# Performance work log

Hardware: AMD Instinct MI355X
Metric: run time of the kernel (lower is better)

The kernel has to match this reference:

```python
import jax, jax.numpy as jnp
import numpy as np

B = 8192
N_INPUT = 64
N_OUTPUT = 128
N_HIDDEN = 32
N_TARGETS = 2
N_EXOGS = 3
N_SERIES = N_TARGETS + N_EXOGS  # 5


def _init_linear(k, fan_in, w_shape, b_shape):
    # torch nn.Linear default init: U(-1/sqrt(fan_in), 1/sqrt(fan_in))
    bound = 1.0 / np.sqrt(fan_in)
    kw, kb = jax.random.split(k)
    W = jax.random.uniform(kw, w_shape, jnp.float32, -bound, bound)
    b = jax.random.uniform(kb, b_shape, jnp.float32, -bound, bound)
    return W, b


def setup_inputs() -> dict:
    key = jax.random.key(0)
    ks = jax.random.split(key, 5)
    target = jax.random.normal(ks[0], (B, N_INPUT, N_TARGETS), jnp.float32)
    exog = jax.random.normal(ks[1], (B, N_INPUT + N_OUTPUT, N_EXOGS), jnp.float32)
    # linear1: (n_input*n_series) -> n_targets
    W1, b1 = _init_linear(ks[2], N_INPUT * N_SERIES, (N_TARGETS, N_INPUT * N_SERIES), (N_TARGETS,))
    # linear2: n_series separate (n_input -> n_hidden) linears, stacked
    W2, b2 = _init_linear(ks[3], N_INPUT, (N_SERIES, N_HIDDEN, N_INPUT), (N_SERIES, N_HIDDEN))
    # linear3: (n_hidden*n_series) -> n_targets
    W3, b3 = _init_linear(ks[4], N_HIDDEN * N_SERIES, (N_TARGETS, N_HIDDEN * N_SERIES), (N_TARGETS,))
    return dict(target=target, exog=exog, W1=W1, b1=b1, W2=W2, b2=b2, W3=W3, b3=b3)


def _single_predict(window, ex, W1, b1, W2, b2, W3, b3):
    # window: (B, n_input, n_targets), ex: (B, n_input, n_exogs)
    te = jnp.concatenate([window, ex], axis=2)  # (B, n_input, n_series)
    flat = te.reshape(te.shape[0], -1)          # time-major, series fastest (torch Flatten order)
    out1 = flat @ W1.T + b1                     # (B, n_targets)
    # per-series tiny linears batched via einsum: h[b,i,:] = W2[i] @ te[b,:,i]
    h = jnp.einsum('bti,iht->bih', te, W2) + b2  # (B, n_series, n_hidden)
    h = jax.nn.sigmoid(h).reshape(h.shape[0], -1)  # series-major concat order matches torch.cat
    out2 = h @ W3.T + b3                        # (B, n_targets)
    return out1 + out2 + window[:, -1, :]


def reference(target, exog, W1, b1, W2, b2, W3, b3):
    def step(window, i):
        ex = jax.lax.dynamic_slice_in_dim(exog, i, N_INPUT, axis=1)  # (B, n_input, n_exogs)
        pred = _single_predict(window, ex, W1, b1, W2, b2, W3, b3)   # (B, n_targets)
        window = jnp.concatenate([window[:, 1:, :], pred[:, None, :]], axis=1)
        return window, pred

    _, preds = jax.lax.scan(step, target, jnp.arange(N_OUTPUT))
    return jnp.transpose(preds, (1, 0, 2))  # (B, n_output, n_targets)
```

## Files before the change

### kernel.cpp

```cpp
#include <hip/hip_runtime.h>
#include <math.h>

#define NB 8192
#define NIN 64
#define NOUT 128
#define NHID 32
#define NEXO 3
#define EXROWS 192
#define NTGT 2

typedef float f32x2 __attribute__((ext_vector_type(2)));
typedef float f32x4 __attribute__((ext_vector_type(4)));
typedef int   i32x4 __attribute__((ext_vector_type(4)));
typedef short bf16x8 __attribute__((ext_vector_type(8)));

#define WS_W2A  0
#define WS_W2BH 12288
#define WS_W2BL 20480
#define WS_WP   28672

__device__ __forceinline__ float sigmoidf(float x) {
    return 1.0f / (1.0f + __expf(-x));
}

__device__ __forceinline__ unsigned short f2bf(float x) {
    unsigned int u = __float_as_uint(x);
    unsigned int r = u + 0x7fffu + ((u >> 16) & 1u);
    return (unsigned short)(r >> 16);
}
__device__ __forceinline__ float bf2f(unsigned short h) {
    return __uint_as_float((unsigned int)h << 16);
}

template<int CTRL>
__device__ __forceinline__ float dpp_add(float x) {
    int p = __builtin_amdgcn_update_dpp(0, __float_as_int(x), CTRL, 0xf, 0xf, true);
    return x + __int_as_float(p);
}

#if __has_builtin(__builtin_amdgcn_permlane16_swap)
__device__ __forceinline__ f32x2 xchg16(f32x2 v, int s) {
    auto rx = __builtin_amdgcn_permlane16_swap(__float_as_uint(v.x), __float_as_uint(v.x), false, false);
    auto ry = __builtin_amdgcn_permlane16_swap(__float_as_uint(v.y), __float_as_uint(v.y), false, false);
    f32x2 r;
    r.x = s ? __uint_as_float(rx[0]) : __uint_as_float(rx[1]);
    r.y = s ? __uint_as_float(ry[0]) : __uint_as_float(ry[1]);
    return r;
}
#else
__device__ __forceinline__ f32x2 xchg16(f32x2 v, int s) {
    (void)s;
    f32x2 r;
    r.x = __int_as_float(__builtin_amdgcn_ds_swizzle(__float_as_int(v.x), 0x401f));
    r.y = __int_as_float(__builtin_amdgcn_ds_swizzle(__float_as_int(v.y), 0x401f));
    return r;
}
#endif

__device__ __forceinline__ f32x2 fold32(f32x2 v, int s32) {
    auto rx = __builtin_amdgcn_permlane32_swap(__float_as_uint(v.x), __float_as_uint(v.x), false, false);
    auto ry = __builtin_amdgcn_permlane32_swap(__float_as_uint(v.y), __float_as_uint(v.y), false, false);
    f32x2 o;
    o.x = v.x + (s32 ? __uint_as_float(rx[0]) : __uint_as_float(rx[1]));
    o.y = v.y + (s32 ? __uint_as_float(ry[0]) : __uint_as_float(ry[1]));
    return o;
}

__global__ __launch_bounds__(256) void narx_prepack_kernel(
    const float* __restrict__ W1, const float* __restrict__ W2,
    const float* __restrict__ W3, const float* __restrict__ b2,
    unsigned char* __restrict__ ws)
{
    const int tid = threadIdx.x;
    unsigned short* w2a  = (unsigned short*)(ws + WS_W2A);
    unsigned short* w2bh = (unsigned short*)(ws + WS_W2BH);
    unsigned short* w2bl = (unsigned short*)(ws + WS_W2BL);
    float* wp = (float*)(ws + WS_WP);

    for (int idx = tid; idx < 6144; idx += 256) {
        int rem = idx;
        int j = rem & 7;  rem >>= 3;
        int lg = rem & 3; rem >>= 2;
        int col = rem & 15; rem >>= 4;
        int kt = rem & 1; rem >>= 1;
        int mt = rem & 1; rem >>= 1;
        int e = rem;
        int row = 64 + e * 32 + mt * 16 + col;
        int t = kt * 32 + lg * 8 + j;
        w2a[idx] = f2bf(W2[(size_t)row * NIN + t]);
    }
    for (int idx = tid; idx < 4096; idx += 256) {
        int rem = idx;
        int j = rem & 7;   rem >>= 3;
        int k0g = rem & 3; rem >>= 2;
        int m0 = rem & 15; rem >>= 4;
        int kt = rem & 1;  rem >>= 1;
        int mt = rem;
        int row = mt * 16 + m0;
        int t = kt * 32 + k0g * 8 + j;
        float x = W2[(size_t)row * NIN + t];
        unsigned short hi = f2bf(x);
        w2bh[idx] = hi;
        w2bl[idx] = f2bf(x - bf2f(hi));
    }
    for (int idx = tid; idx < 384; idx += 256) {
        int e = idx >> 7;
        int r = idx & 127;
        int t = r >> 1, o = r & 1;
        wp[idx] = W1[o * 320 + t * 5 + 2 + e];
    }
    if (tid < 192) wp[384 + tid] = W3[(tid / 96) * 160 + 64 + (tid % 96)];
    if (tid < 96)  wp[576 + tid] = b2[64 + tid];
}

__global__ __launch_bounds__(256, 4) void narx_exog_kernel(
    const float* __restrict__ exog,
    const float* __restrict__ b1, const float* __restrict__ b3,
    const unsigned char* __restrict__ ws,
    float* __restrict__ E)
{
    __shared__ __align__(16) float exs[NEXO][EXROWS];
    __shared__ __align__(16) unsigned short exrep[NEXO * 8][200];
    __shared__ __align__(16) float2 w1e2[NEXO][NIN];
    __shared__ __align__(16) float w3l[2][96];
    __shared__ __align__(16) float b2l[96];

    const unsigned short* w2a = (const unsigned short*)(ws + WS_W2A);
    const float* wp = (const float*)(ws + WS_WP);

    const int tid = threadIdx.x;
    const int b = blockIdx.x;
    const float* exb = exog + (size_t)b * (EXROWS * NEXO);

    for (int idx = tid; idx < EXROWS * NEXO; idx += 256) {
        int t = idx / 3;
        int e = idx - t * 3;
        exs[e][t] = exb[idx];
    }
    for (int idx = tid; idx < 384; idx += 256) ((float*)w1e2)[idx] = wp[idx];
    if (tid < 192) ((float*)w3l)[tid] = wp[384 + tid];
    if (tid < 96)  b2l[tid] = wp[576 + tid];
    __syncthreads();

    for (int idx = tid; idx < NEXO * 8 * 192; idx += 256) {
        int e = idx / 1536;
        int rem = idx - e * 1536;
        int r = rem / 192;
        int q = rem - r * 192;
        float v = (q + r < 192) ? exs[e][q + r] : 0.f;
        exrep[e * 8 + r][q] = f2bf(v);
    }
    __syncthreads();

    const int wv = tid >> 6;
    const int l  = tid & 63;
    const int iw = wv * 32;
    const int lg = l >> 4;
    const int col = l & 15;

    float acc0[2] = {0.f, 0.f};
    float acc1[2] = {0.f, 0.f};

    #pragma unroll 1
    for (int e = 0; e < NEXO; ++e) {
        f32x4 b2v[2], w30v[2], w31v[2];
        #pragma unroll
        for (int mt = 0; mt < 2; ++mt) {
            b2v[mt]  = *(const f32x4*)&b2l[e * 32 + mt * 16 + lg * 4];
            w30v[mt] = *(const f32x4*)&w3l[0][e * 32 + mt * 16 + lg * 4];
            w31v[mt] = *(const f32x4*)&w3l[1][e * 32 + mt * 16 + lg * 4];
        }

        f32x4 cacc[2][2];
        #pragma unroll
        for (int mt = 0; mt < 2; ++mt)
            #pragma unroll
            for (int nt = 0; nt < 2; ++nt)
                cacc[mt][nt] = b2v[mt];

        #pragma unroll
        for (int kt = 0; kt < 2; ++kt) {
            bf16x8 af[2], bfr[2];
            #pragma unroll
            for (int mt = 0; mt < 2; ++mt)
                af[mt] = *(const bf16x8*)(w2a + ((size_t)((e * 2 + mt) * 2 + kt)) * 512
                                              + col * 32 + lg * 8);
            #pragma unroll
            for (int nt = 0; nt < 2; ++nt)
                bfr[nt] = *(const bf16x8*)&exrep[e * 8 + (l & 7)]
                              [iw + nt * 16 + kt * 32 + lg * 8 + ((l >> 3) & 1) * 8];
            #pragma unroll
            for (int mt = 0; mt < 2; ++mt)
                #pragma unroll
                for (int nt = 0; nt < 2; ++nt)
                    cacc[mt][nt] = __builtin_amdgcn_mfma_f32_16x16x32_bf16(
                        af[mt], bfr[nt], cacc[mt][nt], 0, 0, 0);
        }

        #pragma unroll
        for (int mt = 0; mt < 2; ++mt)
            #pragma unroll
            for (int nt = 0; nt < 2; ++nt) {
                #pragma unroll
                for (int r = 0; r < 4; ++r) {
                    float sg = sigmoidf(cacc[mt][nt][r]);
                    acc0[nt] += w30v[mt][r] * sg;
                    acc1[nt] += w31v[mt][r] * sg;
                }
            }

        const float* exs_e = &exs[e][0];
        #pragma unroll
        for (int dt = 0; dt < 16; ++dt) {
            float2 wv2 = w1e2[e][lg * 16 + dt];
            float x0 = exs_e[iw + l + dt];
            float x1 = exs_e[iw + 16 + l + dt];
            acc0[0] += wv2.x * x0;
            acc1[0] += wv2.y * x0;
            acc0[1] += wv2.x * x1;
            acc1[1] += wv2.y * x1;
        }
    }

    #pragma unroll
    for (int nt = 0; nt < 2; ++nt) {
        acc0[nt] += __shfl_xor(acc0[nt], 16, 64);
        acc0[nt] += __shfl_xor(acc0[nt], 32, 64);
        acc1[nt] += __shfl_xor(acc1[nt], 16, 64);
        acc1[nt] += __shfl_xor(acc1[nt], 32, 64);
    }
    if (lg == 0) {
        const float bias0 = b1[0] + b3[0];
        const float bias1 = b1[1] + b3[1];
        #pragma unroll
        for (int nt = 0; nt < 2; ++nt) {
            int i = iw + nt * 16 + col;
            *(float2*)&E[(size_t)b * (NOUT * NTGT) + i * 2] =
                make_float2(acc0[nt] + bias0, acc1[nt] + bias1);
        }
    }
}

#define CH 8
#define NCH 16

__global__ __launch_bounds__(64) void narx_recur_kernel(
    const float* __restrict__ target,
    const float* __restrict__ W1,
    const float* __restrict__ W2, const float* __restrict__ b2,
    const float* __restrict__ W3,
    const unsigned char* __restrict__ ws,
    float* __restrict__ out)
{
    __shared__ __align__(16) f32x2 yw[NTGT][EXROWS];
    __shared__ __align__(16) unsigned int ypk[NTGT][2][200];
    __shared__ __align__(16) f32x2 ew[NTGT][NOUT];
    __shared__ __align__(16) float pt[64][20];

    const unsigned short* w2bh = (const unsigned short*)(ws + WS_W2BH);
    const unsigned short* w2bl = (const unsigned short*)(ws + WS_W2BL);

    const int l = threadIdx.x;
    const int s   = (l >> 4) & 1;
    const int h   = (l & 15) | ((l >> 5) << 4);
    const int u   = s * NHID + h;
    const int s32 = (l >> 5) & 1;
    const size_t bA = (size_t)blockIdx.x * 2;
    const size_t bB = bA + 1;

    for (int i = l; i < NTGT * 2 * 200; i += 64) ((unsigned int*)ypk)[i] = 0u;

    {
        float4 eA = *(const float4*)&out[bA * (NOUT * NTGT) + l * 4];
        float4 eB = *(const float4*)&out[bB * (NOUT * NTGT) + l * 4];
        ew[0][2 * l]     = f32x2{eA.x, eB.x};
        ew[1][2 * l]     = f32x2{eA.y, eB.y};
        ew[0][2 * l + 1] = f32x2{eA.z, eB.z};
        ew[1][2 * l + 1] = f32x2{eA.w, eB.w};
    }
    {
        float2 tA = *(const float2*)&target[bA * (NIN * NTGT) + l * 2];
        float2 tB = *(const float2*)&target[bB * (NIN * NTGT) + l * 2];
        yw[0][l] = f32x2{tA.x, tB.x};
        yw[1][l] = f32x2{tA.y, tB.y};
        float v[2][2] = {{tA.x, tB.x}, {tA.y, tB.y}};
        #pragma unroll
        for (int ss = 0; ss < 2; ++ss)
            #pragma unroll
            for (int q = 0; q < 2; ++q) {
                unsigned short hi = f2bf(v[ss][q]);
                unsigned short lo = f2bf(v[ss][q] - bf2f(hi));
                ypk[ss][q][l] = (unsigned int)hi | ((unsigned int)lo << 16);
            }
    }

    bf16x8 ahf[4][2], alf[4][2];
    {
        const int m0 = l & 15, k0g = l >> 4;
        #pragma unroll
        for (int mt = 0; mt < 4; ++mt)
            #pragma unroll
            for (int kt = 0; kt < 2; ++kt) {
                const int off = ((mt * 2 + kt) * 16 + m0) * 32 + k0g * 8;
                ahf[mt][kt] = *(const bf16x8*)(w2bh + off);
                alf[mt][kt] = *(const bf16x8*)(w2bl + off);
            }
    }

    const float bb    = b2[u];
    const float w3own = W3[s * 160 + u];
    const float w3oth = W3[(1 - s) * 160 + u];
    const float wo1a  = W1[s * 320 + (2 * h) * 5 + s];
    const float wo1b  = W1[s * 320 + (2 * h + 1) * 5 + s];
    const float wo2a  = W1[(1 - s) * 320 + (2 * h) * 5 + s];
    const float wo2b  = W1[(1 - s) * 320 + (2 * h + 1) * 5 + s];
    float w2t[7];
    #pragma unroll
    for (int j = 0; j < 7; ++j) w2t[j] = W2[(size_t)u * NIN + 57 + j];

    f32x2* Y = &yw[s][0];
    const f32x2* EV = &ew[s][0];

    const int lag = l & 7;
    const int qb  = (l >> 3) & 1;
    const int bk0 = (l >> 4) * 8;
    const unsigned int* pk0 = &ypk[0][qb][0];
    const unsigned int* pk1 = &ypk[1][qb][0];

    #pragma unroll 1
    for (int c = 0; c < NCH; ++c) {
        const int i0 = c * CH;

        if (c > 0 && l < 16) {
            const int ss = l >> 3, j = l & 7;
            const int row = i0 + 56 + j;
            f32x2 v = yw[ss][row];
            unsigned short hA = f2bf(v.x);
            unsigned short hB = f2bf(v.y);
            ypk[ss][0][row] = (unsigned int)hA | ((unsigned int)f2bf(v.x - bf2f(hA)) << 16);
            ypk[ss][1][row] = (unsigned int)hB | ((unsigned int)f2bf(v.y - bf2f(hB)) << 16);
        }

        f32x4 acc[4];
        #pragma unroll
        for (int mt = 0; mt < 4; ++mt) acc[mt] = f32x4{0.f, 0.f, 0.f, 0.f};

        #pragma unroll
        for (int kt = 0; kt < 2; ++kt) {
            const int base = i0 + lag + bk0 + kt * 32;
            unsigned int r0[8], r1[8];
            #pragma unroll
            for (int j = 0; j < 8; ++j) { r0[j] = pk0[base + j]; r1[j] = pk1[base + j]; }
            i32x4 h0, l0, h1, l1;
            #pragma unroll
            for (int j2 = 0; j2 < 4; ++j2) {
                h0[j2] = (int)__builtin_amdgcn_perm(r0[2*j2+1], r0[2*j2], 0x05040100u);
                l0[j2] = (int)__builtin_amdgcn_perm(r0[2*j2+1], r0[2*j2], 0x07060302u);
                h1[j2] = (int)__builtin_amdgcn_perm(r1[2*j2+1], r1[2*j2], 0x05040100u);
                l1[j2] = (int)__builtin_amdgcn_perm(r1[2*j2+1], r1[2*j2], 0x07060302u);
            }
            const bf16x8 bh0 = __builtin_bit_cast(bf16x8, h0);
            const bf16x8 bl0 = __builtin_bit_cast(bf16x8, l0);
            const bf16x8 bh1 = __builtin_bit_cast(bf16x8, h1);
            const bf16x8 bl1 = __builtin_bit_cast(bf16x8, l1);
            #pragma unroll
            for (int mt = 0; mt < 4; ++mt) {
                const bf16x8 bh = (mt < 2) ? bh0 : bh1;
                const bf16x8 bl = (mt < 2) ? bl0 : bl1;
                acc[mt] = __builtin_amdgcn_mfma_f32_16x16x32_bf16(ahf[mt][kt], bh, acc[mt], 0, 0, 0);
                acc[mt] = __builtin_amdgcn_mfma_f32_16x16x32_bf16(ahf[mt][kt], bl, acc[mt], 0, 0, 0);
                acc[mt] = __builtin_amdgcn_mfma_f32_16x16x32_bf16(alf[mt][kt], bh, acc[mt], 0, 0, 0);
            }
        }

        {
            const int n = l & 15, r0w = (l >> 4) * 4;
            #pragma unroll
            for (int mt = 0; mt < 4; ++mt)
                #pragma unroll
                for (int r = 0; r < 4; ++r)
                    pt[mt * 16 + r0w + r][n] = acc[mt][r];
        }
        f32x4 pa = *(const f32x4*)&pt[u][0];
        f32x4 pb = *(const f32x4*)&pt[u][4];
        f32x4 pc = *(const f32x4*)&pt[u][8];
        f32x4 pd = *(const f32x4*)&pt[u][12];
        f32x2 P2[CH];
        #pragma unroll
        for (int ci = 0; ci < 4; ++ci) {
            P2[ci]     = f32x2{pa[ci], pc[ci]} + bb;
            P2[ci + 4] = f32x2{pb[ci], pd[ci]} + bb;
        }

        f32x2 ev8[CH];
        #pragma unroll
        for (int q = 0; q < 4; ++q) {
            f32x4 e4 = *(const f32x4*)&EV[i0 + 2 * q];
            ev8[2 * q]     = f32x2{e4[0], e4[1]};
            ev8[2 * q + 1] = f32x2{e4[2], e4[3]};
        }
        f32x2 predprev = Y[i0 + 63];

        #pragma unroll
        for (int ci = 0; ci < CH; ++ci) {
            const int i = i0 + ci;
            const f32x2 y1a = Y[i + 2 * h];
            const f32x2 y1b = Y[i + 2 * h + 1];

            f32x2 sg;
            sg.x = sigmoidf(P2[ci].x);
            sg.y = sigmoidf(P2[ci].y);

            f32x2 va = w3own * sg + wo1a * y1a + wo1b * y1b;
            f32x2 vb = w3oth * sg + wo2a * y1a + wo2b * y1b;

            f32x2 cc = va + xchg16(vb, s);
            cc.x = dpp_add<0xB1>(cc.x);  cc.y = dpp_add<0xB1>(cc.y);
            cc.x = dpp_add<0x4E>(cc.x);  cc.y = dpp_add<0x4E>(cc.y);
            cc.x = dpp_add<0x141>(cc.x); cc.y = dpp_add<0x141>(cc.y);
            cc.x = dpp_add<0x128>(cc.x); cc.y = dpp_add<0x128>(cc.y);
            cc = fold32(cc, s32);

            const f32x2 pred = cc + ev8[ci] + predprev;

            #pragma unroll
            for (int cj = ci + 1; cj < CH; ++cj)
                P2[cj] += w2t[7 - (cj - ci)] * pred;

            if ((l & 47) == 0) Y[i + NIN] = pred;
            predprev = pred;
        }
    }

    {
        f32x2 a0 = yw[0][NIN + 2 * l];
        f32x2 a1 = yw[1][NIN + 2 * l];
        f32x2 c0 = yw[0][NIN + 2 * l + 1];
        f32x2 c1 = yw[1][NIN + 2 * l + 1];
        *(float4*)&out[bA * (NOUT * NTGT) + l * 4] = make_float4(a0.x, a1.x, c0.x, c1.x);
        *(float4*)&out[bB * (NOUT * NTGT) + l * 4] = make_float4(a0.y, a1.y, c0.y, c1.y);
    }
}

extern "C" void kernel_launch(void* const* d_in, const int* in_sizes, int n_in,
                              void* d_out, int out_size, void* d_ws, size_t ws_size,
                              hipStream_t stream) {
    (void)in_sizes; (void)n_in; (void)out_size; (void)ws_size;
    const float* target = (const float*)d_in[0];
    const float* exog   = (const float*)d_in[1];
    const float* W1     = (const float*)d_in[2];
    const float* b1     = (const float*)d_in[3];
    const float* W2     = (const float*)d_in[4];
    const float* b2     = (const float*)d_in[5];
    const float* W3     = (const float*)d_in[6];
    const float* b3     = (const float*)d_in[7];
    float* out = (float*)d_out;
    unsigned char* ws = (unsigned char*)d_ws;

    hipLaunchKernelGGL(narx_prepack_kernel, dim3(1), dim3(256), 0, stream,
                       W1, W2, W3, b2, ws);
    hipLaunchKernelGGL(narx_exog_kernel, dim3(NB), dim3(256), 0, stream,
                       exog, b1, b3, ws, out);
    hipLaunchKernelGGL(narx_recur_kernel, dim3(NB / 2), dim3(64), 0, stream,
                       target, W1, W2, b2, W3, ws, out);
}
```

Measured before the change: 211.2 us.

## Issue next chunk's MFMA projection before the serial recurrence, correcting stale rows

The hidden-layer MFMA for chunk c+1 is now issued at the start of chunk c, before that chunk's predictions exist, so matrix work can overlap the serial per-step recurrence. The window rows that are still stale (predictions made during chunk c) are accounted for by accumulating corr terms with an extended 15-tap slice of W2 during the recurrence, then added when P2 is rebuilt. This costs extra FMAs per step, more registers, and a reordered LDS write/read of pt and ypk, which could create hazards.

```diff
diff --git a/kernel.cpp b/kernel.cpp
--- a/kernel.cpp
+++ b/kernel.cpp
@@ -314,9 +314,9 @@
     const float wo1b  = W1[s * 320 + (2 * h + 1) * 5 + s];
     const float wo2a  = W1[(1 - s) * 320 + (2 * h) * 5 + s];
     const float wo2b  = W1[(1 - s) * 320 + (2 * h + 1) * 5 + s];
-    float w2t[7];
+    float w2x[15];
     #pragma unroll
-    for (int j = 0; j < 7; ++j) w2t[j] = W2[(size_t)u * NIN + 57 + j];
+    for (int j = 0; j < 15; ++j) w2x[j] = W2[(size_t)u * NIN + 49 + j];
 
     f32x2* Y = &yw[s][0];
     const f32x2* EV = &ew[s][0];
@@ -326,6 +326,61 @@
     const int bk0 = (l >> 4) * 8;
     const unsigned int* pk0 = &ypk[0][qb][0];
     const unsigned int* pk1 = &ypk[1][qb][0];
+
+    auto mfma_to_pt = [&](const int i0m) {
+        f32x4 acc[4];
+        #pragma unroll
+        for (int mt = 0; mt < 4; ++mt) acc[mt] = f32x4{0.f, 0.f, 0.f, 0.f};
+        #pragma unroll
+        for (int kt = 0; kt < 2; ++kt) {
+            const int base = i0m + lag + bk0 + kt * 32;
+            unsigned int r0[8], r1[8];
+            #pragma unroll
+            for (int j = 0; j < 8; ++j) { r0[j] = pk0[base + j]; r1[j] = pk1[base + j]; }
+            i32x4 h0v, l0v, h1v, l1v;
+            #pragma unroll
+            for (int j2 = 0; j2 < 4; ++j2) {
+                h0v[j2] = (int)__builtin_amdgcn_perm(r0[2*j2+1], r0[2*j2], 0x05040100u);
+                l0v[j2] = (int)__builtin_amdgcn_perm(r0[2*j2+1], r0[2*j2], 0x07060302u);
+                h1v[j2] = (int)__builtin_amdgcn_perm(r1[2*j2+1], r1[2*j2], 0x05040100u);
+                l1v[j2] = (int)__builtin_amdgcn_perm(r1[2*j2+1], r1[2*j2], 0x07060302u);
+            }
+            const bf16x8 bh0 = __builtin_bit_cast(bf16x8, h0v);
+            const bf16x8 bl0 = __builtin_bit_cast(bf16x8, l0v);
+            const bf16x8 bh1 = __builtin_bit_cast(bf16x8, h1v);
+            const bf16x8 bl1 = __builtin_bit_cast(bf16x8, l1v);
+            #pragma unroll
+            for (int mt = 0; mt < 4; ++mt) {
+                const bf16x8 bh = (mt < 2) ? bh0 : bh1;
+                const bf16x8 bl = (mt < 2) ? bl0 : bl1;
+                acc[mt] = __builtin_amdgcn_mfma_f32_16x16x32_bf16(ahf[mt][kt], bh, acc[mt], 0, 0, 0);
+                acc[mt] = __builtin_amdgcn_mfma_f32_16x16x32_bf16(ahf[mt][kt], bl, acc[mt], 0, 0, 0);
+                acc[mt] = __builtin_amdgcn_mfma_f32_16x16x32_bf16(alf[mt][kt], bh, acc[mt], 0, 0, 0);
+            }
+        }
+        const int n = l & 15, r0w = (l >> 4) * 4;
+        #pragma unroll
+        for (int mt = 0; mt < 4; ++mt)
+            #pragma unroll
+            for (int r = 0; r < 4; ++r)
+                pt[mt * 16 + r0w + r][n] = acc[mt][r];
+    };
+
+    f32x2 P2[CH], corr[CH];
+    mfma_to_pt(0);
+    {
+        f32x4 pa = *(const f32x4*)&pt[u][0];
+        f32x4 pb = *(const f32x4*)&pt[u][4];
+        f32x4 pc = *(const f32x4*)&pt[u][8];
+        f32x4 pd = *(const f32x4*)&pt[u][12];
+        #pragma unroll
+        for (int ci = 0; ci < 4; ++ci) {
+            P2[ci]     = f32x2{pa[ci], pc[ci]} + bb;
+            P2[ci + 4] = f32x2{pb[ci], pd[ci]} + bb;
+        }
+    }
+    #pragma unroll
+    for (int j = 0; j < CH; ++j) corr[j] = f32x2{0.f, 0.f};
 
     #pragma unroll 1
     for (int c = 0; c < NCH; ++c) {
@@ -341,56 +396,7 @@
             ypk[ss][1][row] = (unsigned int)hB | ((unsigned int)f2bf(v.y - bf2f(hB)) << 16);
         }
 
-        f32x4 acc[4];
-        #pragma unroll
-        for (int mt = 0; mt < 4; ++mt) acc[mt] = f32x4{0.f, 0.f, 0.f, 0.f};
-
-        #pragma unroll
-        for (int kt = 0; kt < 2; ++kt) {
-            const int base = i0 + lag + bk0 + kt * 32;
-            unsigned int r0[8], r1[8];
-            #pragma unroll
-            for (int j = 0; j < 8; ++j) { r0[j] = pk0[base + j]; r1[j] = pk1[base + j]; }
-            i32x4 h0, l0, h1, l1;
-            #pragma unroll
-            for (int j2 = 0; j2 < 4; ++j2) {
-                h0[j2] = (int)__builtin_amdgcn_perm(r0[2*j2+1], r0[2*j2], 0x05040100u);
-                l0[j2] = (int)__builtin_amdgcn_perm(r0[2*j2+1], r0[2*j2], 0x07060302u);
-                h1[j2] = (int)__builtin_amdgcn_perm(r1[2*j2+1], r1[2*j2], 0x05040100u);
-                l1[j2] = (int)__builtin_amdgcn_perm(r1[2*j2+1], r1[2*j2], 0x07060302u);
-            }
-            const bf16x8 bh0 = __builtin_bit_cast(bf16x8, h0);
-            const bf16x8 bl0 = __builtin_bit_cast(bf16x8, l0);
-            const bf16x8 bh1 = __builtin_bit_cast(bf16x8, h1);
-            const bf16x8 bl1 = __builtin_bit_cast(bf16x8, l1);
-            #pragma unroll
-            for (int mt = 0; mt < 4; ++mt) {
-                const bf16x8 bh = (mt < 2) ? bh0 : bh1;
-                const bf16x8 bl = (mt < 2) ? bl0 : bl1;
-                acc[mt] = __builtin_amdgcn_mfma_f32_16x16x32_bf16(ahf[mt][kt], bh, acc[mt], 0, 0, 0);
-                acc[mt] = __builtin_amdgcn_mfma_f32_16x16x32_bf16(ahf[mt][kt], bl, acc[mt], 0, 0, 0);
-                acc[mt] = __builtin_amdgcn_mfma_f32_16x16x32_bf16(alf[mt][kt], bh, acc[mt], 0, 0, 0);
-            }
-        }
-
-        {
-            const int n = l & 15, r0w = (l >> 4) * 4;
-            #pragma unroll
-            for (int mt = 0; mt < 4; ++mt)
-                #pragma unroll
-                for (int r = 0; r < 4; ++r)
-                    pt[mt * 16 + r0w + r][n] = acc[mt][r];
-        }
-        f32x4 pa = *(const f32x4*)&pt[u][0];
-        f32x4 pb = *(const f32x4*)&pt[u][4];
-        f32x4 pc = *(const f32x4*)&pt[u][8];
-        f32x4 pd = *(const f32x4*)&pt[u][12];
-        f32x2 P2[CH];
-        #pragma unroll
-        for (int ci = 0; ci < 4; ++ci) {
-            P2[ci]     = f32x2{pa[ci], pc[ci]} + bb;
-            P2[ci + 4] = f32x2{pb[ci], pd[ci]} + bb;
-        }
+        if (c + 1 < NCH) mfma_to_pt(i0 + CH);
 
         f32x2 ev8[CH];
         #pragma unroll
@@ -425,10 +431,27 @@
 
             #pragma unroll
             for (int cj = ci + 1; cj < CH; ++cj)
-                P2[cj] += w2t[7 - (cj - ci)] * pred;
+                P2[cj] += w2x[15 - (cj - ci)] * pred;
+            #pragma unroll
+            for (int cin = 0; cin < CH; ++cin)
+                corr[cin] += w2x[7 + ci - cin] * pred;
 
             if ((l & 47) == 0) Y[i + NIN] = pred;
             predprev = pred;
+        }
+
+        if (c + 1 < NCH) {
+            f32x4 pa = *(const f32x4*)&pt[u][0];
+            f32x4 pb = *(const f32x4*)&pt[u][4];
+            f32x4 pc = *(const f32x4*)&pt[u][8];
+            f32x4 pd = *(const f32x4*)&pt[u][12];
+            #pragma unroll
+            for (int ci = 0; ci < 4; ++ci) {
+                P2[ci]     = f32x2{pa[ci], pc[ci]} + bb + corr[ci];
+                P2[ci + 4] = f32x2{pb[ci], pd[ci]} + bb + corr[ci + 4];
+            }
+            #pragma unroll
+            for (int j = 0; j < CH; ++j) corr[j] = f32x2{0.f, 0.f};
         }
     }
 
```

New measurement: 203.3 us. 1.04x faster.
